# Kernel tuning notes

Hardware: AMD Instinct MI355X
Metric: run time of the kernel (lower is better)

## Reference

```python
import math
import jax, jax.numpy as jnp
import numpy as np

NUM_HEADS = 16

def setup_inputs() -> dict:
    key = jax.random.key(0)
    k1, k2, k3, k4, k5 = jax.random.split(key, 5)
    B, S, D = 8, 4096, 1024
    x = jax.random.normal(k1, (B, S, D), dtype=jnp.float32)
    W_qkv = jax.random.normal(k2, (D, 3 * D), dtype=jnp.float32) * (1.0 / math.sqrt(D))
    b_qkv = jax.random.normal(k3, (3 * D,), dtype=jnp.float32) * 0.02
    W_out = jax.random.normal(k4, (D, D), dtype=jnp.float32) * (1.0 / math.sqrt(D))
    b_out = jax.random.normal(k5, (D,), dtype=jnp.float32) * 0.02
    return {"x": x, "W_qkv": W_qkv, "b_qkv": b_qkv, "W_out": W_out, "b_out": b_out}

def reference(x, W_qkv, b_qkv, W_out, b_out):
    B, S, D = x.shape
    H = NUM_HEADS
    hd = D // H
    scale = 1.0 / math.sqrt(hd)
    # QKV projection: (B,S,D) -> (B,S,3D), reshaped to (B,S,H,3*hd)
    qkv = (x @ W_qkv + b_qkv).reshape(B, S, H, 3 * hd)
    q, k, v = jnp.split(qkv, 3, axis=-1)  # each (B,S,H,hd)
    # Faithful to source: no head permute, so attention is across the H heads
    # at each (batch, seq) position. scores: (B,S,H,H)
    scores = jnp.einsum('bsqd,bskd->bsqk', q, k) * scale
    attn = jax.nn.softmax(scores, axis=-1)
    values = jnp.einsum('bsqk,bskd->bsqd', attn, v).reshape(B, S, D)
    return values @ W_out + b_out
```

## Files before the change

kernel.cpp:

```cpp
#include <hip/hip_runtime.h>
#include <hip/hip_bf16.h>

#define TOKENS   32768
#define DMODEL   1024
#define THREE_D  3072

using u16 = unsigned short;
typedef __attribute__((ext_vector_type(8))) short short8;
typedef __attribute__((ext_vector_type(4))) float f32x4;

__device__ __forceinline__ float bf2f(u16 u) {
  union { unsigned int i; float f; } v; v.i = ((unsigned int)u) << 16; return v.f;
}
__device__ __forceinline__ u16 f2bf(float f) {
  __hip_bfloat16 h = __float2bfloat16(f);
  return *reinterpret_cast<u16*>(&h);
}

__device__ __forceinline__ void gload_lds16(const u16* g, u16* l) {
  __builtin_amdgcn_global_load_lds((const __attribute__((address_space(1))) void*)g,
                                   (__attribute__((address_space(3))) void*)l,
                                   16, 0, 0);
}

__global__ __launch_bounds__(256) void convert_f32_bf16(const float* __restrict__ in,
                                                        u16* __restrict__ out, long n) {
  long i = ((long)blockIdx.x * 256 + threadIdx.x) * 4;
  if (i >= n) return;
  float4 v = *reinterpret_cast<const float4*>(in + i);
  ushort4 o;
  o.x = f2bf(v.x); o.y = f2bf(v.y); o.z = f2bf(v.z); o.w = f2bf(v.w);
  *reinterpret_cast<ushort4*>(out + i) = o;
}

__global__ __launch_bounds__(256) void transpose_convert(const float* __restrict__ in,
                                                         u16* __restrict__ out,
                                                         int R, int C) {
  __shared__ u16 tile[32][33];
  const int bc = blockIdx.x * 32;
  const int br = blockIdx.y * 32;
  const int tx = threadIdx.x & 31;
  const int ty = threadIdx.x >> 5;
  #pragma unroll
  for (int i = 0; i < 32; i += 8)
    tile[ty + i][tx] = f2bf(in[(long)(br + ty + i) * C + bc + tx]);
  __syncthreads();
  #pragma unroll
  for (int i = 0; i < 32; i += 8)
    out[(long)(bc + ty + i) * R + br + tx] = tile[tx][ty + i];
}

#define BM 256
#define BN 256
#define BK 64

#define VM4 asm volatile("s_waitcnt vmcnt(4)" ::: "memory")
#define VM6 asm volatile("s_waitcnt vmcnt(6)" ::: "memory")
#define VM0 asm volatile("s_waitcnt vmcnt(0)" ::: "memory")
#define VMN ((void)0)
#define NOSTAGE ((void)0)

#define STAGE_A(T, H)                                                          \
  { _Pragma("unroll") for (int j_ = 0; j_ < 2; j_++) {                         \
      const int lr_ = (H) * 128 + (wave * 2 + j_) * 8;                         \
      gload_lds16(A + (long)(bm + lr_ + sr) * a_stride + (long)(T) * a_grp + scol, \
                  &As[(T) & 1][lr_ * BK]);                                     \
  } }
#define STAGE_B(T, H)                                                          \
  { _Pragma("unroll") for (int j_ = 0; j_ < 2; j_++) {                         \
      const int lr_ = (H) * 128 + (wave * 2 + j_) * 8;                         \
      gload_lds16(BT + (long)(bn + lr_ + sr) * K + (T) * BK + scol,            \
                  &Bs[(T) & 1][lr_ * BK]);                                     \
  } }

#define READ_A(BUF, QR)                                                        \
  { _Pragma("unroll") for (int mi = 0; mi < 2; mi++)                           \
      _Pragma("unroll") for (int kh = 0; kh < 2; kh++)                         \
        a[mi][kh] = *reinterpret_cast<const short8*>(                          \
            &As[BUF][((QR) * 128 + wrow + mi * 16 + lrow) * BK +               \
                     (((kh * 4 + quad) ^ xs) * 8)]); }
#define READ_B(BUF, QC)                                                        \
  { _Pragma("unroll") for (int ni = 0; ni < 4; ni++)                           \
      _Pragma("unroll") for (int kh = 0; kh < 2; kh++)                         \
        b[ni][kh] = *reinterpret_cast<const short8*>(                          \
            &Bs[BUF][((QC) * 128 + wcol + ni * 16 + lrow) * BK +               \
                     (((kh * 4 + quad) ^ xs) * 8)]); }

#define REGION(QR, QC, STAGE, READS, VMW)                                      \
  {                                                                            \
    __builtin_amdgcn_sched_barrier(0);                                         \
    __builtin_amdgcn_s_barrier();                                              \
    asm volatile("s_waitcnt lgkmcnt(0)" ::: "memory");                         \
    __builtin_amdgcn_sched_barrier(0);                                         \
    __builtin_amdgcn_s_setprio(1);                                             \
    _Pragma("unroll") for (int mi = 0; mi < 2; mi++)                           \
      _Pragma("unroll") for (int ni = 0; ni < 4; ni++) {                       \
        acc[QR][QC][mi][ni] = __builtin_amdgcn_mfma_f32_16x16x32_bf16(         \
            a[mi][0], b[ni][0], acc[QR][QC][mi][ni], 0, 0, 0);                 \
        acc[QR][QC][mi][ni] = __builtin_amdgcn_mfma_f32_16x16x32_bf16(         \
            a[mi][1], b[ni][1], acc[QR][QC][mi][ni], 0, 0, 0);                 \
      }                                                                        \
    __builtin_amdgcn_s_setprio(0);                                             \
    STAGE;                                                                     \
    READS;                                                                     \
    VMW;                                                                       \
  }

template <bool OUT_F32>
__global__ __launch_bounds__(512, 2) void gemm_bt_bias(
    const u16* __restrict__ A, const u16* __restrict__ BT,
    const float* __restrict__ bias, void* __restrict__ Cv,
    int M, int N, int K, long a_stride, int a_grp) {
  __shared__ alignas(16) u16 As[2][BM * BK];
  __shared__ alignas(16) u16 Bs[2][BN * BK];
  (void)M;

  const int cpx = gridDim.x >> 3;
  const int wg  = ((int)blockIdx.x & 7) * cpx + ((int)blockIdx.x >> 3);
  const int tiles_n = N / BN;
  const int bm = (wg / tiles_n) * BM;
  const int bn = (wg % tiles_n) * BN;

  const int tid  = threadIdx.x;
  const int wave = tid >> 6;
  const int lane = tid & 63;
  const int wrow = (wave & 3) * 32;
  const int wcol = (wave >> 2) * 64;
  const int lrow = lane & 15;
  const int quad = lane >> 4;
  const int xs   = lrow & 7;

  const int sr     = lane >> 3;
  const int schunk = (lane & 7) ^ sr;
  const int scol   = schunk * 8;

  const int NT = K / BK;

  f32x4 acc[2][2][2][4];
  #pragma unroll
  for (int i = 0; i < 2; i++)
    #pragma unroll
    for (int j = 0; j < 2; j++)
      #pragma unroll
      for (int m = 0; m < 2; m++)
        #pragma unroll
        for (int n = 0; n < 4; n++) acc[i][j][m][n] = (f32x4){0.f, 0.f, 0.f, 0.f};

  STAGE_A(0, 0); STAGE_B(0, 0); STAGE_A(0, 1); STAGE_B(0, 1);
  STAGE_B(1, 0); STAGE_A(1, 1); STAGE_B(1, 1);
  VM6;
  __builtin_amdgcn_s_barrier();

  short8 a[2][2];
  short8 b[4][2];
  READ_A(0, 0);
  READ_B(0, 0);

  #pragma unroll 1
  for (int t = 0; t + 3 < NT; t += 2) {
    REGION(0, 0, STAGE_A(t + 1, 0), READ_A(0, 1),              VMN);
    REGION(1, 0, STAGE_B(t + 2, 0), READ_B(0, 1),              VMN);
    REGION(1, 1, STAGE_A(t + 2, 1), READ_A(0, 0),              VM4);
    REGION(0, 1, STAGE_B(t + 2, 1), { READ_A(1, 0) READ_B(1, 0) }, VMN);
    REGION(0, 0, STAGE_A(t + 2, 0), READ_A(1, 1),              VMN);
    REGION(1, 0, STAGE_B(t + 3, 0), READ_B(1, 1),              VMN);
    REGION(1, 1, STAGE_A(t + 3, 1), READ_A(1, 0),              VM4);
    REGION(0, 1, STAGE_B(t + 3, 1), { READ_A(0, 0) READ_B(0, 0) }, VMN);
  }
  REGION(0, 0, STAGE_A(NT - 1, 0), READ_A(0, 1),               VMN);
  REGION(1, 0, NOSTAGE,            READ_B(0, 1),               VMN);
  REGION(1, 1, NOSTAGE,            READ_A(0, 0),               VM0);
  REGION(0, 1, NOSTAGE,            { READ_A(1, 0) READ_B(1, 0) }, VMN);
  REGION(0, 0, NOSTAGE,            READ_A(1, 1),               VMN);
  REGION(1, 0, NOSTAGE,            READ_B(1, 1),               VMN);
  REGION(1, 1, NOSTAGE,            READ_A(1, 0),               VMN);
  REGION(0, 1, NOSTAGE,            NOSTAGE,                    VMN);

  #pragma unroll
  for (int qc = 0; qc < 2; qc++) {
    #pragma unroll
    for (int ni = 0; ni < 4; ni++) {
      const int col = bn + qc * 128 + wcol + ni * 16 + lrow;
      const float bv = bias[col];
      #pragma unroll
      for (int qr = 0; qr < 2; qr++) {
        #pragma unroll
        for (int mi = 0; mi < 2; mi++) {
          #pragma unroll
          for (int r = 0; r < 4; r++) {
            const int row = bm + qr * 128 + wrow + mi * 16 + quad * 4 + r;
            const float val = acc[qr][qc][mi][ni][r] + bv;
            if (OUT_F32)
              ((float*)Cv)[(long)row * N + col] = val;
            else
              ((u16*)Cv)[(long)row * N + col] = f2bf(val);
          }
        }
      }
    }
  }
}

__global__ __launch_bounds__(256) void attn_local(u16* __restrict__ qkv) {
  __shared__ float p_s[4][16][16];
  const int tid  = threadIdx.x;
  const int wave = tid >> 6;
  const int lane = tid & 63;
  const int t    = blockIdx.x * 4 + wave;
  u16* row = qkv + (long)t * THREE_D;
  const int lrow = lane & 15;
  const int quad = lane >> 4;
  const int kq   = quad * 8;

  short8 a0 = *reinterpret_cast<const short8*>(row + lrow * 192 + kq);
  short8 a1 = *reinterpret_cast<const short8*>(row + lrow * 192 + 32 + kq);
  short8 b0 = *reinterpret_cast<const short8*>(row + lrow * 192 + 64 + kq);
  short8 b1 = *reinterpret_cast<const short8*>(row + lrow * 192 + 96 + kq);
  f32x4 s = {0.f, 0.f, 0.f, 0.f};
  s = __builtin_amdgcn_mfma_f32_16x16x32_bf16(a0, b0, s, 0, 0, 0);
  s = __builtin_amdgcn_mfma_f32_16x16x32_bf16(a1, b1, s, 0, 0, 0);

  const float scale = 0.125f;
  float p[4];
  #pragma unroll
  for (int r = 0; r < 4; r++) {
    float x = s[r] * scale;
    float m = x;
    #pragma unroll
    for (int mask = 1; mask < 16; mask <<= 1) m = fmaxf(m, __shfl_xor(m, mask));
    float e = __expf(x - m);
    float l = e;
    #pragma unroll
    for (int mask = 1; mask < 16; mask <<= 1) l += __shfl_xor(l, mask);
    p[r] = e / l;
  }
  #pragma unroll
  for (int r = 0; r < 4; r++) p_s[wave][quad * 4 + r][lrow] = p[r];
  __syncthreads();

  float o[16];
  #pragma unroll
  for (int i = 0; i < 16; i++) o[i] = 0.f;
  #pragma unroll
  for (int j = 0; j < 16; j++) {
    float vj = bf2f(row[j * 192 + 128 + lane]);
    #pragma unroll
    for (int i = 0; i < 16; i++) o[i] += p_s[wave][i][j] * vj;
  }
  #pragma unroll
  for (int i = 0; i < 16; i++)
    row[i * 192 + lane] = f2bf(o[i]);
}

extern "C" void kernel_launch(void* const* d_in, const int* in_sizes, int n_in,
                              void* d_out, int out_size, void* d_ws, size_t ws_size,
                              hipStream_t stream) {
  const float* x     = (const float*)d_in[0];
  const float* W_qkv = (const float*)d_in[1];
  const float* b_qkv = (const float*)d_in[2];
  const float* W_out = (const float*)d_in[3];
  const float* b_out = (const float*)d_in[4];
  float* out = (float*)d_out;

  char* ws = (char*)d_ws;
  u16* qkv   = (u16*)ws;  ws += (size_t)TOKENS * THREE_D * 2;
  u16* x_bf  = (u16*)ws;  ws += (size_t)TOKENS * DMODEL * 2;
  u16* wqkvT = (u16*)ws;  ws += (size_t)THREE_D * DMODEL * 2;
  u16* woutT = (u16*)ws;

  dim3 tb(256);
  dim3 gtb(512);
  convert_f32_bf16<<<dim3((TOKENS * DMODEL) / 1024), tb, 0, stream>>>(
      x, x_bf, (long)TOKENS * DMODEL);
  transpose_convert<<<dim3(THREE_D / 32, DMODEL / 32), tb, 0, stream>>>(W_qkv, wqkvT, DMODEL, THREE_D);
  transpose_convert<<<dim3(DMODEL / 32, DMODEL / 32), tb, 0, stream>>>(W_out, woutT, DMODEL, DMODEL);
  gemm_bt_bias<false><<<dim3((TOKENS / BM) * (THREE_D / BN)), gtb, 0, stream>>>(
      x_bf, wqkvT, b_qkv, qkv, TOKENS, THREE_D, DMODEL, (long)DMODEL, 64);
  attn_local<<<dim3(TOKENS / 4), tb, 0, stream>>>(qkv);
  gemm_bt_bias<true><<<dim3((TOKENS / BM) * (DMODEL / BN)), gtb, 0, stream>>>(
      qkv, woutT, b_out, out, TOKENS, DMODEL, DMODEL, (long)THREE_D, 192);
}
```

Measured before the change: 617.4 us.

## Double-buffer GEMM fragment registers so LDS reads overlap MFMA per region

Restructures the GEMM main loop so that A/B fragment registers are double-buffered. Each region issues the next region's LDS reads before the MFMAs and waits with partial lgkmcnt counts instead of lgkmcnt(0), letting LDS reads overlap matrix math. The global-to-LDS staging schedule also changes: a whole tile's A or B halves are staged together and vmcnt waits become full drains, with a one-tile prefetch prologue instead of nearly two tiles. This costs more VGPRs for fragments, at occupancy 2, and the vmcnt(0) waits may expose global latency.

```diff
diff --git a/kernel.cpp b/kernel.cpp
--- a/kernel.cpp
+++ b/kernel.cpp
@@ -54,11 +54,12 @@
 #define BN 256
 #define BK 64
 
-#define VM4 asm volatile("s_waitcnt vmcnt(4)" ::: "memory")
-#define VM6 asm volatile("s_waitcnt vmcnt(6)" ::: "memory")
-#define VM0 asm volatile("s_waitcnt vmcnt(0)" ::: "memory")
-#define VMN ((void)0)
-#define NOSTAGE ((void)0)
+#define LGKM(N) { asm volatile("s_waitcnt lgkmcnt(" #N ")" ::: "memory"); \
+                  __builtin_amdgcn_sched_barrier(0); }
+#define VMW0  asm volatile("s_waitcnt vmcnt(0)" ::: "memory")
+#define BARR  { __builtin_amdgcn_sched_barrier(0); __builtin_amdgcn_s_barrier(); \
+                __builtin_amdgcn_sched_barrier(0); }
+#define NOOP  ((void)0)
 
 #define STAGE_A(T, H)                                                          \
   { _Pragma("unroll") for (int j_ = 0; j_ < 2; j_++) {                         \
@@ -73,38 +74,29 @@
                   &Bs[(T) & 1][lr_ * BK]);                                     \
   } }
 
-#define READ_A(BUF, QR)                                                        \
+#define RDA(AS, BUF, QR)                                                       \
   { _Pragma("unroll") for (int mi = 0; mi < 2; mi++)                           \
       _Pragma("unroll") for (int kh = 0; kh < 2; kh++)                         \
-        a[mi][kh] = *reinterpret_cast<const short8*>(                          \
+        a[AS][mi][kh] = *reinterpret_cast<const short8*>(                      \
             &As[BUF][((QR) * 128 + wrow + mi * 16 + lrow) * BK +               \
                      (((kh * 4 + quad) ^ xs) * 8)]); }
-#define READ_B(BUF, QC)                                                        \
+#define RDB(BS, BUF, QC)                                                       \
   { _Pragma("unroll") for (int ni = 0; ni < 4; ni++)                           \
       _Pragma("unroll") for (int kh = 0; kh < 2; kh++)                         \
-        b[ni][kh] = *reinterpret_cast<const short8*>(                          \
+        b[BS][ni][kh] = *reinterpret_cast<const short8*>(                      \
             &Bs[BUF][((QC) * 128 + wcol + ni * 16 + lrow) * BK +               \
                      (((kh * 4 + quad) ^ xs) * 8)]); }
 
-#define REGION(QR, QC, STAGE, READS, VMW)                                      \
-  {                                                                            \
-    __builtin_amdgcn_sched_barrier(0);                                         \
-    __builtin_amdgcn_s_barrier();                                              \
-    asm volatile("s_waitcnt lgkmcnt(0)" ::: "memory");                         \
-    __builtin_amdgcn_sched_barrier(0);                                         \
-    __builtin_amdgcn_s_setprio(1);                                             \
+#define MMA16(QR, QC, AS, BS)                                                  \
+  { __builtin_amdgcn_s_setprio(1);                                             \
     _Pragma("unroll") for (int mi = 0; mi < 2; mi++)                           \
       _Pragma("unroll") for (int ni = 0; ni < 4; ni++) {                       \
         acc[QR][QC][mi][ni] = __builtin_amdgcn_mfma_f32_16x16x32_bf16(         \
-            a[mi][0], b[ni][0], acc[QR][QC][mi][ni], 0, 0, 0);                 \
+            a[AS][mi][0], b[BS][ni][0], acc[QR][QC][mi][ni], 0, 0, 0);         \
         acc[QR][QC][mi][ni] = __builtin_amdgcn_mfma_f32_16x16x32_bf16(         \
-            a[mi][1], b[ni][1], acc[QR][QC][mi][ni], 0, 0, 0);                 \
+            a[AS][mi][1], b[BS][ni][1], acc[QR][QC][mi][ni], 0, 0, 0);         \
       }                                                                        \
-    __builtin_amdgcn_s_setprio(0);                                             \
-    STAGE;                                                                     \
-    READS;                                                                     \
-    VMW;                                                                       \
-  }
+    __builtin_amdgcn_s_setprio(0); }
 
 template <bool OUT_F32>
 __global__ __launch_bounds__(512, 2) void gemm_bt_bias(
@@ -146,35 +138,34 @@
         #pragma unroll
         for (int n = 0; n < 4; n++) acc[i][j][m][n] = (f32x4){0.f, 0.f, 0.f, 0.f};
 
-  STAGE_A(0, 0); STAGE_B(0, 0); STAGE_A(0, 1); STAGE_B(0, 1);
-  STAGE_B(1, 0); STAGE_A(1, 1); STAGE_B(1, 1);
-  VM6;
+  STAGE_A(0, 0); STAGE_A(0, 1); STAGE_B(0, 0); STAGE_B(0, 1);
+  VMW0;
   __builtin_amdgcn_s_barrier();
 
-  short8 a[2][2];
-  short8 b[4][2];
-  READ_A(0, 0);
-  READ_B(0, 0);
+  short8 a[2][2][2];
+  short8 b[2][4][2];
+  RDA(0, 0, 0);
+  RDB(0, 0, 0);
 
   #pragma unroll 1
   for (int t = 0; t + 3 < NT; t += 2) {
-    REGION(0, 0, STAGE_A(t + 1, 0), READ_A(0, 1),              VMN);
-    REGION(1, 0, STAGE_B(t + 2, 0), READ_B(0, 1),              VMN);
-    REGION(1, 1, STAGE_A(t + 2, 1), READ_A(0, 0),              VM4);
-    REGION(0, 1, STAGE_B(t + 2, 1), { READ_A(1, 0) READ_B(1, 0) }, VMN);
-    REGION(0, 0, STAGE_A(t + 2, 0), READ_A(1, 1),              VMN);
-    REGION(1, 0, STAGE_B(t + 3, 0), READ_B(1, 1),              VMN);
-    REGION(1, 1, STAGE_A(t + 3, 1), READ_A(1, 0),              VM4);
-    REGION(0, 1, STAGE_B(t + 3, 1), { READ_A(0, 0) READ_B(0, 0) }, VMN);
-  }
-  REGION(0, 0, STAGE_A(NT - 1, 0), READ_A(0, 1),               VMN);
-  REGION(1, 0, NOSTAGE,            READ_B(0, 1),               VMN);
-  REGION(1, 1, NOSTAGE,            READ_A(0, 0),               VM0);
-  REGION(0, 1, NOSTAGE,            { READ_A(1, 0) READ_B(1, 0) }, VMN);
-  REGION(0, 0, NOSTAGE,            READ_A(1, 1),               VMN);
-  REGION(1, 0, NOSTAGE,            READ_B(1, 1),               VMN);
-  REGION(1, 1, NOSTAGE,            READ_A(1, 0),               VMN);
-  REGION(0, 1, NOSTAGE,            NOSTAGE,                    VMN);
+    BARR; RDA(1, 0, 1);             STAGE_A(t + 1, 0); STAGE_A(t + 1, 1); LGKM(4);  MMA16(0, 0, 0, 0);
+    BARR; RDB(1, 0, 1);             STAGE_B(t + 1, 0); STAGE_B(t + 1, 1); LGKM(8);  MMA16(1, 0, 1, 0);
+    BARR; RDA(0, 0, 0);                                                   LGKM(4);  MMA16(1, 1, 1, 1); VMW0;
+    BARR; RDA(1, 1, 0); RDB(0, 1, 0);                                     LGKM(12); MMA16(0, 1, 0, 1);
+    BARR; RDA(0, 1, 1);             STAGE_A(t + 2, 0); STAGE_A(t + 2, 1); LGKM(4);  MMA16(0, 0, 1, 0);
+    BARR; RDB(1, 1, 1);             STAGE_B(t + 2, 0); STAGE_B(t + 2, 1); LGKM(8);  MMA16(1, 0, 0, 0);
+    BARR; RDA(1, 1, 0);                                                   LGKM(4);  MMA16(1, 1, 0, 1); VMW0;
+    BARR; RDA(0, 0, 0); RDB(0, 0, 0);                                     LGKM(12); MMA16(0, 1, 1, 1);
+  }
+  BARR; RDA(1, 0, 1);               STAGE_A(NT - 1, 0); STAGE_A(NT - 1, 1); LGKM(4);  MMA16(0, 0, 0, 0);
+  BARR; RDB(1, 0, 1);               STAGE_B(NT - 1, 0); STAGE_B(NT - 1, 1); LGKM(8);  MMA16(1, 0, 1, 0);
+  BARR; RDA(0, 0, 0);                                                       LGKM(4);  MMA16(1, 1, 1, 1); VMW0;
+  BARR; RDA(1, 1, 0); RDB(0, 1, 0);                                         LGKM(12); MMA16(0, 1, 0, 1);
+  BARR; RDA(0, 1, 1);                                                       LGKM(4);  MMA16(0, 0, 1, 0);
+  BARR; RDB(1, 1, 1);                                                       LGKM(8);  MMA16(1, 0, 0, 0);
+  BARR; RDA(1, 1, 0);                                                       LGKM(4);  MMA16(1, 1, 0, 1);
+  BARR;                                                                     LGKM(0);  MMA16(0, 1, 1, 1);
 
   #pragma unroll
   for (int qc = 0; qc < 2; qc++) {
```

After: 891.7 us. 44.4% more time.
